# Kernel tuning notes

Hardware: AMD Instinct MI355X
Metric: run time of the kernel (lower is better)

Reference implementation:

```python
import jax, jax.numpy as jnp
import numpy as np

NUM_TOKENS = 1024  # codebook size (n_embed)
CODE_DIM = 256     # embedding_dim
BETA = 0.25


def setup_inputs() -> dict:
    key = jax.random.key(0)
    k1, k2 = jax.random.split(key)
    z = jax.random.normal(k1, (64, 512, CODE_DIM), dtype=jnp.float32)
    weight = jax.random.normal(k2, (NUM_TOKENS, CODE_DIM), dtype=jnp.float32)
    return {"z": z, "weight": weight}


def reference(z, weight):
    # z: [B, T, D]; weight: [K, D]
    z_flat = z.reshape(-1, CODE_DIM)                       # [N, D]
    # squared euclidean distances: ||z||^2 + ||w||^2 - 2 z.w
    d = (jnp.sum(z_flat ** 2, axis=1, keepdims=True)
         + jnp.sum(weight ** 2, axis=1)
         - 2.0 * jnp.matmul(z_flat, weight.T))             # [N, K]
    min_encoding_indices = jnp.argmin(d, axis=1)           # [N]
    z_q = weight[min_encoding_indices].reshape(z.shape)    # gather

    # perplexity from mean one-hot usage (avoid materializing one-hot via bincount)
    counts = jnp.bincount(min_encoding_indices, length=NUM_TOKENS)
    e_mean = counts.astype(z.dtype) / z_flat.shape[0]
    perplexity = jnp.exp(-jnp.sum(e_mean * jnp.log(e_mean + 1e-10)))

    # commitment loss (codebook is EMA-updated, so z_q is detached)
    loss = BETA * jnp.mean((jax.lax.stop_gradient(z_q) - z) ** 2)
    # straight-through estimator
    z_q_st = z + jax.lax.stop_gradient(z_q - z)
    return (loss, z_q_st, min_encoding_indices, perplexity)
```

## Files before the change

kernel.cpp:

```cpp
#include <hip/hip_runtime.h>

#define N_TOKENS 32768
#define K_CODES  1024
#define DIM      256
#define BETA     0.25f

typedef unsigned long long u64;
typedef _Float16 half8 __attribute__((ext_vector_type(8)));
typedef float floatx4 __attribute__((ext_vector_type(4)));

__global__ void init_kernel(const float* __restrict__ w, float* __restrict__ wn,
                            int* __restrict__ counts, u64* __restrict__ keys,
                            _Float16* __restrict__ whiG, _Float16* __restrict__ wloG) {
    int k = blockIdx.x;
    int lane = threadIdx.x;
    float4 v = *(const float4*)(w + (size_t)k * DIM + lane * 4);
    float vals[4] = {v.x, v.y, v.z, v.w};
    float s = 0.f;
    #pragma unroll
    for (int e = 0; e < 4; e++) {
        s += vals[e] * vals[e];
        _Float16 h = (_Float16)vals[e];
        whiG[k * DIM + lane * 4 + e] = h;
        wloG[k * DIM + lane * 4 + e] = (_Float16)(vals[e] - (float)h);
    }
    #pragma unroll
    for (int off = 32; off; off >>= 1) s += __shfl_down(s, off);
    if (lane == 0) { wn[k] = s; counts[k] = 0; }
    if (lane < 32) keys[k * 32 + lane] = ~0ull;
}

__global__ __launch_bounds__(256, 2) void argmin_kernel(
    const float* __restrict__ z, const _Float16* __restrict__ whiG,
    const _Float16* __restrict__ wloG, const float* __restrict__ wn,
    u64* __restrict__ keys)
{
    constexpr int ZS = 40;
    __shared__ _Float16 zhi[128 * ZS], zlo[128 * ZS];
    __shared__ _Float16 whi[256 * ZS], wlo[256 * ZS];

    const int tid  = threadIdx.x;
    const int lane = tid & 63;
    const int wid  = tid >> 6;
    const int wm   = wid >> 1;
    const int wq   = wid & 1;
    const int t_   = blockIdx.x & 255;
    const int q    = blockIdx.x >> 8;
    const int tok0  = t_ * 128;
    const int kbase = q * 256;

    float wnr[8];
    #pragma unroll
    for (int j = 0; j < 8; j++)
        wnr[j] = wn[kbase + wq * 128 + j * 16 + (lane & 15)];

    floatx4 acc[4][8];
    #pragma unroll
    for (int i = 0; i < 4; i++)
        #pragma unroll
        for (int j = 0; j < 8; j++)
            acc[i][j] = (floatx4){0.f, 0.f, 0.f, 0.f};

    const int r0 = tid >> 2;
    const int g0 = tid & 3;

    for (int dt = 0; dt < 8; ++dt) {
        const int d0 = dt * 32;
        __syncthreads();

        #pragma unroll
        for (int s = 0; s < 2; s++) {
            int t = r0 + s * 64;
            const float* p = z + (size_t)(tok0 + t) * DIM + d0 + g0 * 8;
            float4 a = *(const float4*)p;
            float4 b = *(const float4*)(p + 4);
            float vals[8] = {a.x, a.y, a.z, a.w, b.x, b.y, b.z, b.w};
            half8 hv, lv;
            #pragma unroll
            for (int e = 0; e < 8; e++) {
                _Float16 h = (_Float16)vals[e];
                hv[e] = h;
                lv[e] = (_Float16)(vals[e] - (float)h);
            }
            *(half8*)&zhi[t * ZS + g0 * 8] = hv;
            *(half8*)&zlo[t * ZS + g0 * 8] = lv;
        }
        #pragma unroll
        for (int s = 0; s < 4; s++) {
            int t = r0 + s * 64;
            size_t goff = (size_t)(kbase + t) * DIM + d0 + g0 * 8;
            *(half8*)&whi[t * ZS + g0 * 8] = *(const half8*)&whiG[goff];
            *(half8*)&wlo[t * ZS + g0 * 8] = *(const half8*)&wloG[goff];
        }
        __syncthreads();

        const int koff = (lane >> 4) * 8;
        half8 ah[4], al[4];
        #pragma unroll
        for (int i = 0; i < 4; i++) {
            int off = (wm * 64 + i * 16 + (lane & 15)) * ZS + koff;
            ah[i] = *(const half8*)&zhi[off];
            al[i] = *(const half8*)&zlo[off];
        }
        __builtin_amdgcn_s_setprio(1);
        #pragma unroll
        for (int j = 0; j < 8; j++) {
            int off = (wq * 128 + j * 16 + (lane & 15)) * ZS + koff;
            half8 bh = *(const half8*)&whi[off];
            half8 bl = *(const half8*)&wlo[off];
            #pragma unroll
            for (int i = 0; i < 4; i++) {
                acc[i][j] = __builtin_amdgcn_mfma_f32_16x16x32_f16(ah[i], bh, acc[i][j], 0, 0, 0);
                acc[i][j] = __builtin_amdgcn_mfma_f32_16x16x32_f16(ah[i], bl, acc[i][j], 0, 0, 0);
                acc[i][j] = __builtin_amdgcn_mfma_f32_16x16x32_f16(al[i], bh, acc[i][j], 0, 0, 0);
            }
        }
        __builtin_amdgcn_s_setprio(0);
    }

    #pragma unroll
    for (int i = 0; i < 4; i++) {
        #pragma unroll
        for (int r = 0; r < 4; r++) {
            float bv = 3.4e38f; int bi = 0;
            #pragma unroll
            for (int j = 0; j < 8; j++) {
                int cl = wq * 128 + j * 16 + (lane & 15);
                float dist = wnr[j] - 2.0f * acc[i][j][r];
                if (dist < bv) { bv = dist; bi = kbase + cl; }
            }
            unsigned uu = __float_as_uint(bv);
            unsigned ss = (uu & 0x80000000u) ? ~uu : (uu | 0x80000000u);
            u64 key = ((u64)ss << 32) | (unsigned)bi;
            #pragma unroll
            for (int m = 1; m < 16; m <<= 1) {
                u64 o = __shfl_xor(key, m);
                if (o < key) key = o;
            }
            if ((lane & 15) == 0) {
                int token = tok0 + wm * 64 + i * 16 + (lane >> 4) * 4 + r;
                atomicMin(&keys[token], key);
            }
        }
    }
}

__global__ void gather_loss_kernel(const float* __restrict__ z,
                                   const float* __restrict__ w,
                                   const u64* __restrict__ keys,
                                   float* __restrict__ zq_out,
                                   float* __restrict__ idxf,
                                   int* __restrict__ counts,
                                   float* __restrict__ partials)
{
    __shared__ float red[4];
    int tid = threadIdx.x;
    int lane = tid & 63;
    int wid = blockIdx.x * 4 + (tid >> 6);
    float s = 0.0f;
    #pragma unroll
    for (int it = 0; it < 4; it++) {
        int tok = wid + it * 8192;
        u64 key = 0;
        if (lane == 0) key = keys[tok];
        key = __shfl(key, 0);
        int k = (int)(key & (u64)(K_CODES - 1));
        float4 wv = *(const float4*)(w + (size_t)k * DIM + lane * 4);
        float4 zv = *(const float4*)(z + (size_t)tok * DIM + lane * 4);
        *(float4*)(zq_out + (size_t)tok * DIM + lane * 4) = wv;
        float dx = wv.x - zv.x, dy = wv.y - zv.y, dz = wv.z - zv.z, dw = wv.w - zv.w;
        s += dx * dx + dy * dy + dz * dz + dw * dw;
        if (lane == 0) {
            idxf[tok] = (float)k;
            atomicAdd(&counts[k], 1);
        }
    }
    #pragma unroll
    for (int off = 32; off; off >>= 1) s += __shfl_down(s, off);
    if (lane == 0) red[tid >> 6] = s;
    __syncthreads();
    if (tid == 0)
        partials[blockIdx.x] = red[0] + red[1] + red[2] + red[3];
}

__global__ void finalize_kernel(const int* __restrict__ counts,
                                const float* __restrict__ partials,
                                float* __restrict__ loss_out,
                                float* __restrict__ ppl_out)
{
    __shared__ float redE[16], redL[16];
    int tid = threadIdx.x;
    float e = (float)counts[tid] * (1.0f / (float)N_TOKENS);
    float t = -e * logf(e + 1e-10f);
    float p = partials[tid] + partials[tid + 1024];
    #pragma unroll
    for (int off = 32; off; off >>= 1) {
        t += __shfl_down(t, off);
        p += __shfl_down(p, off);
    }
    if ((tid & 63) == 0) { redE[tid >> 6] = t; redL[tid >> 6] = p; }
    __syncthreads();
    if (tid == 0) {
        float se = 0.0f, sl = 0.0f;
        #pragma unroll
        for (int i = 0; i < 16; i++) { se += redE[i]; sl += redL[i]; }
        *ppl_out = expf(se);
        *loss_out = BETA * sl / (float)((size_t)N_TOKENS * DIM);
    }
}

extern "C" void kernel_launch(void* const* d_in, const int* in_sizes, int n_in,
                              void* d_out, int out_size, void* d_ws, size_t ws_size,
                              hipStream_t stream) {
    const float* z = (const float*)d_in[0];
    const float* w = (const float*)d_in[1];
    float* out = (float*)d_out;

    float* loss_out = out;
    float* zq_out   = out + 1;
    float* idxf     = out + 1 + (size_t)N_TOKENS * DIM;
    float* ppl_out  = out + (out_size - 1);

    float* wn       = (float*)d_ws;
    int*   counts   = (int*)d_ws + 1024;
    float* partials = (float*)d_ws + 2048;
    u64*   keys     = (u64*)((char*)d_ws + 16384);
    _Float16* whiG  = (_Float16*)((char*)d_ws + 16384 + (size_t)N_TOKENS * 8);
    _Float16* wloG  = whiG + (size_t)K_CODES * DIM;

    init_kernel<<<K_CODES, 64, 0, stream>>>(w, wn, counts, keys, whiG, wloG);
    argmin_kernel<<<4 * 256, 256, 0, stream>>>(z, whiG, wloG, wn, keys);
    gather_loss_kernel<<<2048, 256, 0, stream>>>(z, w, keys, zq_out, idxf, counts, partials);
    finalize_kernel<<<1, 1024, 0, stream>>>(counts, partials, loss_out, ppl_out);
}
```

Baseline: 160.3 us.

## Double-buffer codebook tiles in LDS with swizzle, load z fragments directly to registers

The argmin kernel now double-buffers the fp16 hi/lo codebook tiles in shared memory. Global loads for the next K-slice are issued before the current compute, and the LDS write is placed mid-way through the MFMA loop, which cuts the syncs per iteration from two to one. The padded layout is replaced with an XOR swizzle to avoid bank conflicts. z fragments are loaded straight from global into registers and split into hi/lo per wave, skipping LDS staging. The cost is duplicated z global reads across the two wq waves and more register pressure from the prefetched codebook fragments.

Measured after the change: 168.5 us. 5.2% more time.

```diff
diff --git a/kernel.cpp b/kernel.cpp
--- a/kernel.cpp
+++ b/kernel.cpp
@@ -35,9 +35,7 @@
     const _Float16* __restrict__ wloG, const float* __restrict__ wn,
     u64* __restrict__ keys)
 {
-    constexpr int ZS = 40;
-    __shared__ _Float16 zhi[128 * ZS], zlo[128 * ZS];
-    __shared__ _Float16 whi[256 * ZS], wlo[256 * ZS];
+    __shared__ __attribute__((aligned(16))) char wbuf[2][32768];
 
     const int tid  = threadIdx.x;
     const int lane = tid & 63;
@@ -63,51 +61,59 @@
 
     const int r0 = tid >> 2;
     const int g0 = tid & 3;
+    const int wst = r0 * 64 + ((g0 * 16) ^ ((r0 & 3) << 4));
+    const _Float16* whg = whiG + (size_t)(kbase + r0) * DIM + g0 * 8;
+    const _Float16* wlg = wloG + (size_t)(kbase + r0) * DIM + g0 * 8;
+
+    const int kg = lane >> 4;
+    const int rb = (wq * 128 + (lane & 15)) * 64 + ((kg * 16) ^ ((lane & 3) << 4));
+
+    const float* zA = z + (size_t)(tok0 + wm * 64 + (lane & 15)) * DIM + kg * 8;
+
+    half8 wh[4], wl[4];
+    auto loadw = [&](int dtn) {
+        #pragma unroll
+        for (int s = 0; s < 4; s++) {
+            wh[s] = *(const half8*)(whg + (size_t)s * 64 * DIM + dtn * 32);
+            wl[s] = *(const half8*)(wlg + (size_t)s * 64 * DIM + dtn * 32);
+        }
+    };
+    auto writew = [&](int b) {
+        #pragma unroll
+        for (int s = 0; s < 4; s++) {
+            *(half8*)&wbuf[b][wst + s * 4096]         = wh[s];
+            *(half8*)&wbuf[b][wst + s * 4096 + 16384] = wl[s];
+        }
+    };
+
+    loadw(0); writew(0);
+    __syncthreads();
 
     for (int dt = 0; dt < 8; ++dt) {
-        const int d0 = dt * 32;
-        __syncthreads();
-
-        #pragma unroll
-        for (int s = 0; s < 2; s++) {
-            int t = r0 + s * 64;
-            const float* p = z + (size_t)(tok0 + t) * DIM + d0 + g0 * 8;
+        const int cur = dt & 1;
+        if (dt < 7) loadw(dt + 1);
+
+        half8 ah[4], al[4];
+        #pragma unroll
+        for (int i = 0; i < 4; i++) {
+            const float* p = zA + (size_t)i * 16 * DIM + dt * 32;
             float4 a = *(const float4*)p;
             float4 b = *(const float4*)(p + 4);
             float vals[8] = {a.x, a.y, a.z, a.w, b.x, b.y, b.z, b.w};
-            half8 hv, lv;
             #pragma unroll
             for (int e = 0; e < 8; e++) {
                 _Float16 h = (_Float16)vals[e];
-                hv[e] = h;
-                lv[e] = (_Float16)(vals[e] - (float)h);
-            }
-            *(half8*)&zhi[t * ZS + g0 * 8] = hv;
-            *(half8*)&zlo[t * ZS + g0 * 8] = lv;
-        }
-        #pragma unroll
-        for (int s = 0; s < 4; s++) {
-            int t = r0 + s * 64;
-            size_t goff = (size_t)(kbase + t) * DIM + d0 + g0 * 8;
-            *(half8*)&whi[t * ZS + g0 * 8] = *(const half8*)&whiG[goff];
-            *(half8*)&wlo[t * ZS + g0 * 8] = *(const half8*)&wloG[goff];
-        }
-        __syncthreads();
-
-        const int koff = (lane >> 4) * 8;
-        half8 ah[4], al[4];
-        #pragma unroll
-        for (int i = 0; i < 4; i++) {
-            int off = (wm * 64 + i * 16 + (lane & 15)) * ZS + koff;
-            ah[i] = *(const half8*)&zhi[off];
-            al[i] = *(const half8*)&zlo[off];
-        }
+                ah[i][e] = h;
+                al[i][e] = (_Float16)(vals[e] - (float)h);
+            }
+        }
+
         __builtin_amdgcn_s_setprio(1);
         #pragma unroll
-        for (int j = 0; j < 8; j++) {
-            int off = (wq * 128 + j * 16 + (lane & 15)) * ZS + koff;
-            half8 bh = *(const half8*)&whi[off];
-            half8 bl = *(const half8*)&wlo[off];
+        for (int j = 0; j < 4; j++) {
+            const char* pb = &wbuf[cur][rb + j * 1024];
+            half8 bh = *(const half8*)pb;
+            half8 bl = *(const half8*)(pb + 16384);
             #pragma unroll
             for (int i = 0; i < 4; i++) {
                 acc[i][j] = __builtin_amdgcn_mfma_f32_16x16x32_f16(ah[i], bh, acc[i][j], 0, 0, 0);
@@ -116,6 +122,25 @@
             }
         }
         __builtin_amdgcn_s_setprio(0);
+
+        if (dt < 7) writew(cur ^ 1);
+
+        __builtin_amdgcn_s_setprio(1);
+        #pragma unroll
+        for (int j = 4; j < 8; j++) {
+            const char* pb = &wbuf[cur][rb + j * 1024];
+            half8 bh = *(const half8*)pb;
+            half8 bl = *(const half8*)(pb + 16384);
+            #pragma unroll
+            for (int i = 0; i < 4; i++) {
+                acc[i][j] = __builtin_amdgcn_mfma_f32_16x16x32_f16(ah[i], bh, acc[i][j], 0, 0, 0);
+                acc[i][j] = __builtin_amdgcn_mfma_f32_16x16x32_f16(ah[i], bl, acc[i][j], 0, 0, 0);
+                acc[i][j] = __builtin_amdgcn_mfma_f32_16x16x32_f16(al[i], bh, acc[i][j], 0, 0, 0);
+            }
+        }
+        __builtin_amdgcn_s_setprio(0);
+
+        __syncthreads();
     }
 
     #pragma unroll
```
